# Performance work log

Measured on AMD Instinct MI355X. Metric: run time of the kernel, lower is better.

Reference implementation:

```python
import jax, jax.numpy as jnp
import numpy as np

B, C, H, W = 32, 256, 32, 32
HEADS, DH = 8, 32          # MHA9: num_heads=8, dim_head=32, total_dim=256
TOT = HEADS * DH


def setup_inputs() -> dict:
    key = jax.random.key(0)
    ks = jax.random.split(key, 10)
    s = 0.02
    return {
        "x": jax.random.normal(ks[0], (B, C, H, W), dtype=jnp.float32),
        "Wq": jax.random.normal(ks[1], (TOT, C), dtype=jnp.float32) * s,
        "bq": jnp.zeros((TOT,), dtype=jnp.float32),
        "Wk": jax.random.normal(ks[2], (TOT, C), dtype=jnp.float32) * s,
        "bk": jnp.zeros((TOT,), dtype=jnp.float32),
        "Wv": jax.random.normal(ks[3], (TOT, C), dtype=jnp.float32) * s,
        "bv": jnp.zeros((TOT,), dtype=jnp.float32),
        "Wo": jax.random.normal(ks[4], (C, TOT), dtype=jnp.float32) * s,
        "bo": jnp.zeros((C,), dtype=jnp.float32),
        "gamma": jnp.zeros((1,), dtype=jnp.float32),
    }


def reference(x, Wq, bq, Wk, bk, Wv, bv, Wo, bo, gamma):
    b, c, h, w = x.shape
    S = h * w

    def proj(Wt, bt):
        # 1x1 conv == channel matmul; reshape to (B, heads, S, dh)
        y = jnp.einsum('oc,bchw->bohw', Wt, x) + bt[None, :, None, None]
        return y.reshape(b, HEADS, DH, S).transpose(0, 1, 3, 2)

    q = proj(Wq, bq)
    k = proj(Wk, bk)
    v = proj(Wv, bv)

    scale = 1.0 / jnp.sqrt(jnp.asarray(DH, dtype=x.dtype))
    scores = jnp.einsum('bhsd,bhtd->bhst', q, k) * scale  # [B,h,S,S] full matrix
    weights = jax.nn.softmax(scores, axis=-1)
    o = jnp.einsum('bhst,bhtd->bhsd', weights, v)          # [B,h,S,dh]
    o = o.transpose(0, 1, 3, 2).reshape(b, TOT, h, w)
    o = jnp.einsum('oc,bchw->bohw', Wo, o) + bo[None, :, None, None]
    x_ = gamma * o + x   # inner residual of MultiHeadAttention
    return x + x_        # outer residual of MulAttontion
```

## Files before the change

kernel.cpp:

```cpp
#include <hip/hip_runtime.h>
#include <stdint.h>

typedef unsigned short u16;
typedef unsigned int   u32;
typedef __attribute__((ext_vector_type(8))) short bf16x8;
typedef __attribute__((ext_vector_type(4))) short bf16x4;
typedef __attribute__((ext_vector_type(4))) float f32x4;
typedef __attribute__((ext_vector_type(16))) float f32x16;

#define NT ((size_t)8388608)

__device__ __forceinline__ float bf2f(u16 u) {
  union { float f; u32 i; } v; v.i = ((u32)u) << 16; return v.f;
}
__device__ __forceinline__ u16 f2bf(float f) {
  union { float f; u32 i; } v; v.f = f;
  u32 r = (v.i + 0x7fffu + ((v.i >> 16) & 1u)) >> 16;
  return (u16)r;
}
__device__ __forceinline__ u32 fbits(float f) {
  union { float f; u32 i; } v; v.f = f; return v.i;
}
__device__ __forceinline__ int detect_bf16(const u32* __restrict__ xd) {
  u32 w = xd[threadIdx.x & 63];
  u32 e = (w >> 8) & 0x7fu;
  unsigned long long m = __ballot((e >= 0x38u) && (e <= 0x41u));
  return __popcll(m) > 32;
}
__device__ __forceinline__ void gld16(const void* g, void* l) {
  __builtin_amdgcn_global_load_lds((const __attribute__((address_space(1))) u32*)g,
                                   (__attribute__((address_space(3))) u32*)l, 16, 0, 0);
}

__global__ void __launch_bounds__(256) prologue_kernel(const void* __restrict__ xin,
                                                       u16* __restrict__ xT,
                                                       const void* __restrict__ W0, const void* __restrict__ W1,
                                                       const void* __restrict__ W2, const void* __restrict__ b0,
                                                       const void* __restrict__ b1, const void* __restrict__ b2,
                                                       u16* __restrict__ wdst, float* __restrict__ bdst,
                                                       const void* __restrict__ Wo, const void* __restrict__ bo,
                                                       const void* __restrict__ gm, u16* __restrict__ wodst,
                                                       float* __restrict__ bodst) {
  const int blk = blockIdx.x;
  const int tid = threadIdx.x;
  const int isbf = detect_bf16((const u32*)xin);
  if (blk < 2048) {
    const int s0 = (blk & 15) * 64, c0 = ((blk >> 4) & 3) * 64, b = blk >> 6;
    __shared__ u16 T[64][72];
    if (isbf) {
      const u16* xp = (const u16*)xin;
      for (int t = tid; t < 512; t += 256) {
        int r = t >> 3, off = (t & 7) * 8;
        *(uint4*)&T[r][off] = *(const uint4*)(xp + ((size_t)(b * 256 + c0 + r)) * 1024 + s0 + off);
      }
    } else {
      const float* xp = (const float*)xin;
      for (int t = tid; t < 512; t += 256) {
        int r = t >> 3, off = (t & 7) * 8;
        const float* s = xp + ((size_t)(b * 256 + c0 + r)) * 1024 + s0 + off;
        const float4 a = *(const float4*)s;
        const float4 c = *(const float4*)(s + 4);
        T[r][off + 0] = f2bf(a.x); T[r][off + 1] = f2bf(a.y);
        T[r][off + 2] = f2bf(a.z); T[r][off + 3] = f2bf(a.w);
        T[r][off + 4] = f2bf(c.x); T[r][off + 5] = f2bf(c.y);
        T[r][off + 6] = f2bf(c.z); T[r][off + 7] = f2bf(c.w);
      }
    }
    __syncthreads();
    for (int t = tid; t < 512; t += 256) {
      int r = t >> 3, off = (t & 7) * 8;
      union { u16 h[8]; uint4 v; } pk;
#pragma unroll
      for (int u = 0; u < 8; u++) pk.h[u] = T[off + u][r];
      *(uint4*)(xT + ((size_t)(b * 1024 + s0 + r)) * 256 + c0 + off) = pk.v;
    }
  } else if (blk < 2240) {
    const int g = blk - 2048;
    const int which = g >> 6, bk = g & 63;
    const void* Ws = which == 0 ? W0 : which == 1 ? W1 : W2;
    const void* bs = which == 0 ? b0 : which == 1 ? b1 : b2;
    const int idx = bk * 1024 + tid * 4;
    u16* dst = wdst + which * 65536 + idx;
    if (isbf) {
      *(ushort4*)dst = *(const ushort4*)((const u16*)Ws + idx);
    } else {
      const float4 sv = *(const float4*)((const float*)Ws + idx);
      ushort4 o; o.x = f2bf(sv.x); o.y = f2bf(sv.y); o.z = f2bf(sv.z); o.w = f2bf(sv.w);
      *(ushort4*)dst = o;
    }
    if (bk == 0) {
      bdst[which * 256 + tid] = isbf ? bf2f(((const u16*)bs)[tid]) : ((const float*)bs)[tid];
    }
  } else {
    const int g = blk - 2240;
    const int idx = g * 1024 + tid * 4;
    if (isbf) {
      *(ushort4*)(wodst + idx) = *(const ushort4*)((const u16*)Wo + idx);
    } else {
      const float4 sv = *(const float4*)((const float*)Wo + idx);
      ushort4 o; o.x = f2bf(sv.x); o.y = f2bf(sv.y); o.z = f2bf(sv.z); o.w = f2bf(sv.w);
      *(ushort4*)(wodst + idx) = o;
    }
    if (g == 0) {
      bodst[tid] = isbf ? bf2f(((const u16*)bo)[tid]) : ((const float*)bo)[tid];
      if (tid == 0) bodst[256] = isbf ? bf2f(((const u16*)gm)[0]) : ((const float*)gm)[0];
    }
  }
}

__global__ void __launch_bounds__(256) prep_o(const void* __restrict__ Wo, const void* __restrict__ bo,
                                              const void* __restrict__ gm, u16* __restrict__ wdst,
                                              float* __restrict__ bdst, const u32* __restrict__ xdet) {
  const int isbf = detect_bf16(xdet);
  const int idx = blockIdx.x * 1024 + threadIdx.x * 4;
  if (isbf) {
    *(ushort4*)(wdst + idx) = *(const ushort4*)((const u16*)Wo + idx);
  } else {
    const float4 sv = *(const float4*)((const float*)Wo + idx);
    ushort4 o; o.x = f2bf(sv.x); o.y = f2bf(sv.y); o.z = f2bf(sv.z); o.w = f2bf(sv.w);
    *(ushort4*)(wdst + idx) = o;
  }
  if (blockIdx.x == 0) {
    int t = threadIdx.x;
    bdst[t] = isbf ? bf2f(((const u16*)bo)[t]) : ((const float*)bo)[t];
    if (t == 0) bdst[256] = isbf ? bf2f(((const u16*)gm)[0]) : ((const float*)gm)[0];
  }
}

__global__ void __launch_bounds__(256) qkv_gemm(const u16* __restrict__ xT,
                                                const u16* __restrict__ Wall,
                                                const float* __restrict__ ball,
                                                u16* __restrict__ Qb, u16* __restrict__ Kb,
                                                u16* __restrict__ Vb) {
  const int z = blockIdx.z, b = z / 3, which = z - b * 3;
  const int tid = threadIdx.x, lane = tid & 63, wave = tid >> 6;
  const int quad = lane >> 4, l16 = lane & 15;
  const int wm = wave >> 1, wn = wave & 1;
  const u16* xb = xT + (size_t)b * 262144;
  const u16* W = Wall + which * 65536;
  const int m0 = blockIdx.y * 128;
  const int n0 = blockIdx.x * 128;

  __shared__ u16 Ash[8192], Bsh[8192];
  f32x4 acc[4][4];
#pragma unroll
  for (int i = 0; i < 4; i++)
#pragma unroll
    for (int j = 0; j < 4; j++) acc[i][j] = (f32x4){0.f, 0.f, 0.f, 0.f};

  const int srow = lane >> 3;
  const int sgc = (lane & 7) ^ (srow & 7);
  for (int k0 = 0; k0 < 256; k0 += 64) {
    __syncthreads();
#pragma unroll
    for (int p = 0; p < 4; p++) {
      const int row = p * 32 + wave * 8;
      gld16(W  + (size_t)(m0 + row + srow) * 256 + k0 + sgc * 8, &Ash[row * 64 + lane * 8]);
      gld16(xb + (size_t)(n0 + row + srow) * 256 + k0 + sgc * 8, &Bsh[row * 64 + lane * 8]);
    }
    __syncthreads();
#pragma unroll
    for (int kk = 0; kk < 2; kk++) {
      bf16x8 av[4], bv[4];
      const int rg = (kk * 4 + quad) ^ (l16 & 7);
#pragma unroll
      for (int i = 0; i < 4; i++) av[i] = *(const bf16x8*)&Ash[(wm * 64 + i * 16 + l16) * 64 + rg * 8];
#pragma unroll
      for (int j = 0; j < 4; j++) bv[j] = *(const bf16x8*)&Bsh[(wn * 64 + j * 16 + l16) * 64 + rg * 8];
#pragma unroll
      for (int i = 0; i < 4; i++)
#pragma unroll
        for (int j = 0; j < 4; j++)
          acc[i][j] = __builtin_amdgcn_mfma_f32_16x16x32_bf16(av[i], bv[j], acc[i][j], 0, 0, 0);
    }
  }

  const float* bias = ball + which * 256;
  const float scale = (which == 0) ? 0.25503486f : 1.0f;
#pragma unroll
  for (int i = 0; i < 4; i++) {
#pragma unroll
    for (int j = 0; j < 4; j++) {
      const int mb = m0 + wm * 64 + i * 16 + quad * 4;
      const int n = n0 + wn * 64 + j * 16 + l16;
      if (which < 2) {
        u16* D = (which ? Kb : Qb) + (size_t)b * 262144;
        ushort4 st;
        st.x = f2bf((acc[i][j][0] + bias[mb + 0]) * scale);
        st.y = f2bf((acc[i][j][1] + bias[mb + 1]) * scale);
        st.z = f2bf((acc[i][j][2] + bias[mb + 2]) * scale);
        st.w = f2bf((acc[i][j][3] + bias[mb + 3]) * scale);
        *(ushort4*)(D + (size_t)(mb >> 5) * 32768 + (size_t)n * 32 + (mb & 31)) = st;
      } else {
        u16* D = Vb + (size_t)b * 262144;
#pragma unroll
        for (int r = 0; r < 4; r++) {
          const int m = mb + r;
          D[(size_t)m * 1024 + n] = f2bf(acc[i][j][r] + bias[m]);
        }
      }
    }
  }
}

__global__ void __launch_bounds__(512) attn_kernel(const u16* __restrict__ Q,
                                                   const u16* __restrict__ K,
                                                   const u16* __restrict__ V,
                                                   u16* __restrict__ O) {
  const int blk = blockIdx.x;
  const int qc = blk >> 8, bh = blk & 255;
  const int b = bh >> 3, h = bh & 7;
  const int tid = threadIdx.x, wave = tid >> 6, lane = tid & 63;
  const int hi = lane >> 5, l32 = lane & 31;
  __shared__ __align__(16) u16 Ksh[2][128 * 32];
  __shared__ __align__(16) u16 Vsh[2][32 * 128];
  const u16* Qg = Q + (size_t)b * 262144 + (size_t)h * 32768;
  const u16* Kg = K + (size_t)b * 262144 + (size_t)h * 32768;
  const u16* Vg = V + (size_t)b * 262144 + (size_t)h * 32768;
  const int qw = qc * 256 + wave * 32;

  bf16x8 qf[2];
#pragma unroll
  for (int ks = 0; ks < 2; ks++)
    qf[ks] = *(const bf16x8*)(Qg + (size_t)(qw + l32) * 32 + ks * 16 + hi * 8);

  const int Gg = wave * 64 + lane;
  const int th = Gg >> 3;
  const int uu = (Gg & 7) ^ (th & 7);
  const u16* ksrc = Kg + (size_t)(th * 2 + (uu >> 2)) * 32 + (uu & 3) * 8;
  u16* kdst0 = &Ksh[0][Gg * 8];
  u16* kdst1 = &Ksh[1][Gg * 8];
  const int vd = tid >> 4;
  const u16* vsrc = Vg + (size_t)vd * 1024 + ((tid & 15) ^ (vd & 15)) * 8;
  u16* vdst0 = &Vsh[0][tid * 8];
  u16* vdst1 = &Vsh[1][tid * 8];

  const int kkey = (l32 >> 1) & 7;
  const int kb0 = (l32 >> 1) * 128 + (((((l32 & 1) << 2) | 0 | hi) ^ kkey) << 4);
  const int kb1 = (l32 >> 1) * 128 + (((((l32 & 1) << 2) | 2 | hi) ^ kkey) << 4);
  int vb[4];
#pragma unroll
  for (int tt = 0; tt < 4; tt++) vb[tt] = l32 * 256 + (((l32 & 12) ^ (tt << 2)) << 4);
  const int vm0 = ((l32 & 3) ^ hi) << 4;
  const int vm1 = ((l32 & 3) ^ (2 | hi)) << 4;

  f32x16 oacc;
#pragma unroll
  for (int r = 0; r < 16; r++) oacc[r] = 0.f;
  f32x16 zro;
#pragma unroll
  for (int r = 0; r < 16; r++) zro[r] = 0.f;
  float lsum = 0.f;

  gld16(ksrc, kdst0);
  gld16(vsrc, vdst0);
  __syncthreads();

#pragma unroll 1
  for (int kt = 0; kt < 8; kt++) {
    const int c = kt & 1;
    if (kt < 7) {
      gld16(ksrc + (size_t)(kt + 1) * 4096, c ? kdst0 : kdst1);
      gld16(vsrc + (kt + 1) * 128,          c ? vdst0 : vdst1);
    }
    const char* Kb = (const char*)&Ksh[c][0];
    const char* Vb = (const char*)&Vsh[c][0];
#pragma unroll
    for (int tt = 0; tt < 4; tt++) {
      const bf16x8 kf0 = *(const bf16x8*)(Kb + tt * 2048 + kb0);
      const bf16x8 kf1 = *(const bf16x8*)(Kb + tt * 2048 + kb1);
      const bf16x8 vf0 = *(const bf16x8*)(Vb + vb[tt] + vm0);
      const bf16x8 vf1 = *(const bf16x8*)(Vb + vb[tt] + vm1);
      __builtin_amdgcn_s_setprio(1);
      f32x16 sf = __builtin_amdgcn_mfma_f32_32x32x16_bf16(kf0, qf[0], zro, 0, 0, 0);
      sf = __builtin_amdgcn_mfma_f32_32x32x16_bf16(kf1, qf[1], sf, 0, 0, 0);
      __builtin_amdgcn_s_setprio(0);
      {
        const float p0 = __builtin_amdgcn_exp2f(sf[0]);
        const float p1 = __builtin_amdgcn_exp2f(sf[1]);
        const float p2 = __builtin_amdgcn_exp2f(sf[2]);
        const float p3 = __builtin_amdgcn_exp2f(sf[3]);
        const float p4 = __builtin_amdgcn_exp2f(sf[4]);
        const float p5 = __builtin_amdgcn_exp2f(sf[5]);
        const float p6 = __builtin_amdgcn_exp2f(sf[6]);
        const float p7 = __builtin_amdgcn_exp2f(sf[7]);
        lsum += ((p0 + p1) + (p2 + p3)) + ((p4 + p5) + (p6 + p7));
        u32 wa, wb, wc, wd;
        asm("v_cvt_pk_bf16_f32 %0, %1, %2" : "=v"(wa) : "v"(p0), "v"(p1));
        asm("v_cvt_pk_bf16_f32 %0, %1, %2" : "=v"(wb) : "v"(p2), "v"(p3));
        asm("v_cvt_pk_bf16_f32 %0, %1, %2" : "=v"(wc) : "v"(p4), "v"(p5));
        asm("v_cvt_pk_bf16_f32 %0, %1, %2" : "=v"(wd) : "v"(p6), "v"(p7));
#if __has_builtin(__builtin_amdgcn_permlane32_swap)
        auto s0 = __builtin_amdgcn_permlane32_swap((int)wc, (int)wa, false, false);
        auto s1 = __builtin_amdgcn_permlane32_swap((int)wd, (int)wb, false, false);
        union { int w[4]; bf16x8 v; } pk;
        pk.w[0] = s0[1]; pk.w[1] = s1[1]; pk.w[2] = s0[0]; pk.w[3] = s1[0];
#else
        const u32 xa = __shfl_xor((int)wa, 32), xb = __shfl_xor((int)wb, 32);
        const u32 xc = __shfl_xor((int)wc, 32), xd = __shfl_xor((int)wd, 32);
        union { u32 w[4]; bf16x8 v; } pk;
        pk.w[0] = hi ? xc : wa; pk.w[1] = hi ? xd : wb;
        pk.w[2] = hi ? wc : xa; pk.w[3] = hi ? wd : xb;
#endif
        __builtin_amdgcn_s_setprio(1);
        oacc = __builtin_amdgcn_mfma_f32_32x32x16_bf16(pk.v, vf0, oacc, 0, 0, 0);
        __builtin_amdgcn_s_setprio(0);
      }
      {
        const float p0 = __builtin_amdgcn_exp2f(sf[8]);
        const float p1 = __builtin_amdgcn_exp2f(sf[9]);
        const float p2 = __builtin_amdgcn_exp2f(sf[10]);
        const float p3 = __builtin_amdgcn_exp2f(sf[11]);
        const float p4 = __builtin_amdgcn_exp2f(sf[12]);
        const float p5 = __builtin_amdgcn_exp2f(sf[13]);
        const float p6 = __builtin_amdgcn_exp2f(sf[14]);
        const float p7 = __builtin_amdgcn_exp2f(sf[15]);
        lsum += ((p0 + p1) + (p2 + p3)) + ((p4 + p5) + (p6 + p7));
        u32 wa, wb, wc, wd;
        asm("v_cvt_pk_bf16_f32 %0, %1, %2" : "=v"(wa) : "v"(p0), "v"(p1));
        asm("v_cvt_pk_bf16_f32 %0, %1, %2" : "=v"(wb) : "v"(p2), "v"(p3));
        asm("v_cvt_pk_bf16_f32 %0, %1, %2" : "=v"(wc) : "v"(p4), "v"(p5));
        asm("v_cvt_pk_bf16_f32 %0, %1, %2" : "=v"(wd) : "v"(p6), "v"(p7));
#if __has_builtin(__builtin_amdgcn_permlane32_swap)
        auto s0 = __builtin_amdgcn_permlane32_swap((int)wc, (int)wa, false, false);
        auto s1 = __builtin_amdgcn_permlane32_swap((int)wd, (int)wb, false, false);
        union { int w[4]; bf16x8 v; } pk;
        pk.w[0] = s0[1]; pk.w[1] = s1[1]; pk.w[2] = s0[0]; pk.w[3] = s1[0];
#else
        const u32 xa = __shfl_xor((int)wa, 32), xb = __shfl_xor((int)wb, 32);
        const u32 xc = __shfl_xor((int)wc, 32), xd = __shfl_xor((int)wd, 32);
        union { u32 w[4]; bf16x8 v; } pk;
        pk.w[0] = hi ? xc : wa; pk.w[1] = hi ? xd : wb;
        pk.w[2] = hi ? wc : xa; pk.w[3] = hi ? wd : xb;
#endif
        __builtin_amdgcn_s_setprio(1);
        oacc = __builtin_amdgcn_mfma_f32_32x32x16_bf16(pk.v, vf1, oacc, 0, 0, 0);
        __builtin_amdgcn_s_setprio(0);
      }
    }
    if (kt < 7) __syncthreads();
  }

  lsum += __shfl_xor(lsum, 32);
  const float linv = 1.0f / lsum;
  u16* Og = O + (size_t)(b * 1024 + qw) * 256 + h * 32 + l32;
#pragma unroll
  for (int r = 0; r < 16; r++) {
    const int qo = (r & 3) + 8 * (r >> 2) + 4 * hi;
    const float li = __shfl(linv, qo);
    Og[(size_t)qo * 256] = f2bf(oacc[r] * li);
  }
}

__global__ void __launch_bounds__(256) out_gemm(const u16* __restrict__ WoB,
                                                const float* __restrict__ bg,
                                                const u16* __restrict__ Ob,
                                                const void* __restrict__ xin,
                                                void* __restrict__ outp,
                                                const u32* __restrict__ xdet) {
  const int b = blockIdx.z;
  const int m0 = blockIdx.x * 128;
  const int n0 = blockIdx.y * 64;
  const int tid = threadIdx.x, lane = tid & 63, wave = tid >> 6;
  const int quad = lane >> 4, l16 = lane & 15;
  const int wm = wave >> 1, wn = wave & 1;
  const int isbf = detect_bf16(xdet);
  const u16* Ab = Ob + (size_t)b * 262144;
  __shared__ u16 Ash[2][8192], Bsh[2][4096];
  f32x4 acc[4][2];
#pragma unroll
  for (int i = 0; i < 4; i++)
#pragma unroll
    for (int j = 0; j < 2; j++) acc[i][j] = (f32x4){0.f, 0.f, 0.f, 0.f};

  const int srow = lane >> 3;
  const int sgc = (lane & 7) ^ (srow & 7);

#pragma unroll
  for (int p = 0; p < 4; p++) {
    const int row = p * 32 + wave * 8;
    gld16(Ab + (size_t)(m0 + row + srow) * 256 + sgc * 8, &Ash[0][row * 64 + lane * 8]);
  }
#pragma unroll
  for (int p = 0; p < 2; p++) {
    const int row = p * 32 + wave * 8;
    gld16(WoB + (size_t)(n0 + row + srow) * 256 + sgc * 8, &Bsh[0][row * 64 + lane * 8]);
  }
  __syncthreads();

#pragma unroll
  for (int k = 0; k < 4; k++) {
    const int c = k & 1;
    if (k < 3) {
      const int k0 = (k + 1) * 64;
#pragma unroll
      for (int p = 0; p < 4; p++) {
        const int row = p * 32 + wave * 8;
        gld16(Ab + (size_t)(m0 + row + srow) * 256 + k0 + sgc * 8, &Ash[c ^ 1][row * 64 + lane * 8]);
      }
#pragma unroll
      for (int p = 0; p < 2; p++) {
        const int row = p * 32 + wave * 8;
        gld16(WoB + (size_t)(n0 + row + srow) * 256 + k0 + sgc * 8, &Bsh[c ^ 1][row * 64 + lane * 8]);
      }
    }
#pragma unroll
    for (int kk = 0; kk < 2; kk++) {
      bf16x8 av[4], bv[2];
      const int rg = (kk * 4 + quad) ^ (l16 & 7);
#pragma unroll
      for (int i = 0; i < 4; i++) av[i] = *(const bf16x8*)&Ash[c][(wm * 64 + i * 16 + l16) * 64 + rg * 8];
#pragma unroll
      for (int j = 0; j < 2; j++) bv[j] = *(const bf16x8*)&Bsh[c][(wn * 32 + j * 16 + l16) * 64 + rg * 8];
#pragma unroll
      for (int i = 0; i < 4; i++)
#pragma unroll
        for (int j = 0; j < 2; j++)
          acc[i][j] = __builtin_amdgcn_mfma_f32_16x16x32_bf16(av[i], bv[j], acc[i][j], 0, 0, 0);
    }
    if (k < 3) __syncthreads();
  }

  const float g = bg[256];
#pragma unroll
  for (int i = 0; i < 4; i++) {
#pragma unroll
    for (int j = 0; j < 2; j++) {
      const int mb = m0 + wm * 64 + i * 16 + quad * 4;
      const int n = n0 + wn * 32 + j * 16 + l16;
      const float bc = bg[n];
      const size_t gi = (size_t)b * 262144 + (size_t)n * 1024 + mb;
      if (isbf) {
        const ushort4 xv = *(const ushort4*)((const u16*)xin + gi);
        ushort4 st;
        st.x = f2bf(2.f * bf2f(xv.x) + g * (acc[i][j][0] + bc));
        st.y = f2bf(2.f * bf2f(xv.y) + g * (acc[i][j][1] + bc));
        st.z = f2bf(2.f * bf2f(xv.z) + g * (acc[i][j][2] + bc));
        st.w = f2bf(2.f * bf2f(xv.w) + g * (acc[i][j][3] + bc));
        *(ushort4*)((u16*)outp + gi) = st;
      } else {
        const float4 xv = *(const float4*)((const float*)xin + gi);
        float4 st;
        st.x = 2.f * xv.x + g * (acc[i][j][0] + bc);
        st.y = 2.f * xv.y + g * (acc[i][j][1] + bc);
        st.z = 2.f * xv.z + g * (acc[i][j][2] + bc);
        st.w = 2.f * xv.w + g * (acc[i][j][3] + bc);
        *(float4*)((float*)outp + gi) = st;
      }
    }
  }
}

extern "C" void kernel_launch(void* const* d_in, const int* in_sizes, int n_in,
                              void* d_out, int out_size, void* d_ws, size_t ws_size,
                              hipStream_t stream) {
  const void* x  = d_in[0];
  const void* Wq = d_in[1]; const void* bq = d_in[2];
  const void* Wk = d_in[3]; const void* bk = d_in[4];
  const void* Wv = d_in[5]; const void* bv = d_in[6];
  const void* Wo = d_in[7]; const void* bo = d_in[8];
  const void* gm = d_in[9];

  u16* ws = (u16*)d_ws;
  u16* xT = ws;
  u16* Qb = ws + NT;
  u16* Kb = ws + 2 * NT;
  u16* Vb = ws + 3 * NT;
  u16* Ob = xT;
  const u32* xdet = (const u32*)x;

  u16* WqkvB = (u16*)d_out;
  float* bqkvF = (float*)((u16*)d_out + 196608);

  const bool tail = ws_size >= (size_t)(4 * NT + 66048) * 2;
  u16* WoB = tail ? (ws + 4 * NT) : Qb;
  float* boF = tail ? (float*)(ws + 4 * NT + 65536) : (float*)(Qb + 65536);

  prologue_kernel<<<dim3(tail ? 2304 : 2240), 256, 0, stream>>>(
      x, xT, Wq, Wk, Wv, bq, bk, bv, WqkvB, bqkvF, Wo, bo, gm, WoB, boF);
  qkv_gemm<<<dim3(8, 2, 96), 256, 0, stream>>>(xT, WqkvB, bqkvF, Qb, Kb, Vb);
  attn_kernel<<<dim3(1024), 512, 0, stream>>>(Qb, Kb, Vb, Ob);
  if (!tail) prep_o<<<dim3(64), 256, 0, stream>>>(Wo, bo, gm, WoB, boF, xdet);
  out_gemm<<<dim3(8, 4, 32), 256, 0, stream>>>(WoB, boF, Ob, x, d_out, xdet);
}
```

Before: 189.0 us.

## Double-buffer QKV GEMM shared tiles and halve M tile for more blocks

```diff
diff --git a/kernel.cpp b/kernel.cpp
--- a/kernel.cpp
+++ b/kernel.cpp
@@ -138,50 +138,71 @@
   const int wm = wave >> 1, wn = wave & 1;
   const u16* xb = xT + (size_t)b * 262144;
   const u16* W = Wall + which * 65536;
-  const int m0 = blockIdx.y * 128;
+  const int m0 = blockIdx.y * 64;
   const int n0 = blockIdx.x * 128;
 
-  __shared__ u16 Ash[8192], Bsh[8192];
-  f32x4 acc[4][4];
-#pragma unroll
-  for (int i = 0; i < 4; i++)
+  __shared__ u16 Ash[2][4096], Bsh[2][8192];
+  f32x4 acc[2][4];
+#pragma unroll
+  for (int i = 0; i < 2; i++)
 #pragma unroll
     for (int j = 0; j < 4; j++) acc[i][j] = (f32x4){0.f, 0.f, 0.f, 0.f};
 
   const int srow = lane >> 3;
   const int sgc = (lane & 7) ^ (srow & 7);
-  for (int k0 = 0; k0 < 256; k0 += 64) {
-    __syncthreads();
-#pragma unroll
-    for (int p = 0; p < 4; p++) {
-      const int row = p * 32 + wave * 8;
-      gld16(W  + (size_t)(m0 + row + srow) * 256 + k0 + sgc * 8, &Ash[row * 64 + lane * 8]);
-      gld16(xb + (size_t)(n0 + row + srow) * 256 + k0 + sgc * 8, &Bsh[row * 64 + lane * 8]);
-    }
-    __syncthreads();
+
+#pragma unroll
+  for (int p = 0; p < 2; p++) {
+    const int row = p * 32 + wave * 8;
+    gld16(W + (size_t)(m0 + row + srow) * 256 + sgc * 8, &Ash[0][row * 64 + lane * 8]);
+  }
+#pragma unroll
+  for (int p = 0; p < 4; p++) {
+    const int row = p * 32 + wave * 8;
+    gld16(xb + (size_t)(n0 + row + srow) * 256 + sgc * 8, &Bsh[0][row * 64 + lane * 8]);
+  }
+  __syncthreads();
+
+#pragma unroll
+  for (int k = 0; k < 4; k++) {
+    const int c = k & 1;
+    if (k < 3) {
+      const int k0 = (k + 1) * 64;
+#pragma unroll
+      for (int p = 0; p < 2; p++) {
+        const int row = p * 32 + wave * 8;
+        gld16(W + (size_t)(m0 + row + srow) * 256 + k0 + sgc * 8, &Ash[c ^ 1][row * 64 + lane * 8]);
+      }
+#pragma unroll
+      for (int p = 0; p < 4; p++) {
+        const int row = p * 32 + wave * 8;
+        gld16(xb + (size_t)(n0 + row + srow) * 256 + k0 + sgc * 8, &Bsh[c ^ 1][row * 64 + lane * 8]);
+      }
+    }
 #pragma unroll
     for (int kk = 0; kk < 2; kk++) {
-      bf16x8 av[4], bv[4];
+      bf16x8 av[2], bv[4];
       const int rg = (kk * 4 + quad) ^ (l16 & 7);
 #pragma unroll
-      for (int i = 0; i < 4; i++) av[i] = *(const bf16x8*)&Ash[(wm * 64 + i * 16 + l16) * 64 + rg * 8];
-#pragma unroll
-      for (int j = 0; j < 4; j++) bv[j] = *(const bf16x8*)&Bsh[(wn * 64 + j * 16 + l16) * 64 + rg * 8];
-#pragma unroll
-      for (int i = 0; i < 4; i++)
+      for (int i = 0; i < 2; i++) av[i] = *(const bf16x8*)&Ash[c][(wm * 32 + i * 16 + l16) * 64 + rg * 8];
+#pragma unroll
+      for (int j = 0; j < 4; j++) bv[j] = *(const bf16x8*)&Bsh[c][(wn * 64 + j * 16 + l16) * 64 + rg * 8];
+#pragma unroll
+      for (int i = 0; i < 2; i++)
 #pragma unroll
         for (int j = 0; j < 4; j++)
           acc[i][j] = __builtin_amdgcn_mfma_f32_16x16x32_bf16(av[i], bv[j], acc[i][j], 0, 0, 0);
     }
+    if (k < 3) __syncthreads();
   }
 
   const float* bias = ball + which * 256;
   const float scale = (which == 0) ? 0.25503486f : 1.0f;
 #pragma unroll
-  for (int i = 0; i < 4; i++) {
+  for (int i = 0; i < 2; i++) {
 #pragma unroll
     for (int j = 0; j < 4; j++) {
-      const int mb = m0 + wm * 64 + i * 16 + quad * 4;
+      const int mb = m0 + wm * 32 + i * 16 + quad * 4;
       const int n = n0 + wn * 64 + j * 16 + l16;
       if (which < 2) {
         u16* D = (which ? Kb : Qb) + (size_t)b * 262144;
@@ -478,7 +499,7 @@
 
   prologue_kernel<<<dim3(tail ? 2304 : 2240), 256, 0, stream>>>(
       x, xT, Wq, Wk, Wv, bq, bk, bv, WqkvB, bqkvF, Wo, bo, gm, WoB, boF);
-  qkv_gemm<<<dim3(8, 2, 96), 256, 0, stream>>>(xT, WqkvB, bqkvF, Qb, Kb, Vb);
+  qkv_gemm<<<dim3(8, 4, 96), 256, 0, stream>>>(xT, WqkvB, bqkvF, Qb, Kb, Vb);
   attn_kernel<<<dim3(1024), 512, 0, stream>>>(Qb, Kb, Vb, Ob);
   if (!tail) prep_o<<<dim3(64), 256, 0, stream>>>(Wo, bo, gm, WoB, boF, xdet);
   out_gemm<<<dim3(8, 4, 32), 256, 0, stream>>>(WoB, boF, Ob, x, d_out, xdet);
```

After: 194.0 us. 1.03x slower.
